# Optimization experiments

Hardware: AMD Instinct MI355X
Metric: run time of the kernel (lower is better)

Reference implementation:

```python
import jax, jax.numpy as jnp
import numpy as np

N_WIRES = 8
DIM = 1 << N_WIRES  # 256
ENC_WIRES = [0, 1, 2, 2, 4, 5, 6, 7]  # faithful to source: wire 2 twice, wire 3 skipped

# Precompute composed CNOT-ring permutation: CNOT(0,1),(1,2),...,(6,7),(7,0)
_idx = np.arange(DIM)
_perm = _idx.copy()
for c, t in [(k, k + 1) for k in range(N_WIRES - 1)] + [(N_WIRES - 1, 0)]:
    cbit = (_idx >> (N_WIRES - 1 - c)) & 1
    P = np.where(cbit == 1, _idx ^ (1 << (N_WIRES - 1 - t)), _idx)
    _perm = _perm[P]
CNOT_PERM = jnp.asarray(_perm)
# Pauli-Z sign table per wire: (8, 256)
Z_SIGNS = jnp.asarray(1 - 2 * ((_idx[None, :] >> (N_WIRES - 1 - np.arange(N_WIRES)[:, None])) & 1)).astype(jnp.float32)


def _rx(state, wire, theta):
    """Apply RX(theta) on `wire`. state: (N, 256) complex64, theta: (N,) float."""
    N = state.shape[0]
    s = state.reshape(N, 1 << wire, 2, 1 << (N_WIRES - 1 - wire))
    half = theta * 0.5
    c = jnp.cos(half)[:, None, None]
    sn = jnp.sin(half)[:, None, None]
    a, b = s[:, :, 0, :], s[:, :, 1, :]
    top = c * a - 1j * sn * b
    bot = -1j * sn * a + c * b
    return jnp.stack([top, bot], axis=2).reshape(N, DIM)


def qlayer(tokens, theta):
    """Batched 8-qubit circuit: encoder RX(x_k), trainable RX(theta_w), CNOT ring, <Z_w>.
    tokens: (N, 8) float32 -> (N, 8) float32 expectation values."""
    N = tokens.shape[0]
    state = jnp.zeros((N, DIM), jnp.complex64).at[:, 0].set(1.0)
    for k, w in enumerate(ENC_WIRES):
        state = _rx(state, w, tokens[:, k])
    for w in range(N_WIRES):
        state = _rx(state, w, jnp.broadcast_to(theta[w], (N,)))
    state = state[:, CNOT_PERM]
    probs = state.real ** 2 + state.imag ** 2  # (N, 256)
    return probs @ Z_SIGNS.T  # (N, 8)


def setup_inputs() -> dict:
    key = jax.random.key(0)
    kx, kt = jax.random.split(key)
    x = jax.random.normal(kx, (16, 1024, 8), dtype=jnp.float32)
    theta = jax.random.uniform(kt, (8,), dtype=jnp.float32, minval=0.0, maxval=2.0 * np.pi)
    return {"x": x, "theta": theta}


def reference(x, theta):
    B, S, E = x.shape
    H, dk = 2, E // 2
    tok = x.reshape(B * S, E)
    # Original computes Q, K, V with the SAME shared q_layer on the SAME input,
    # so Q == K == V; compute once.
    qkv = qlayer(tok, theta).reshape(B, S, E)
    h = qkv.reshape(B, S, H, dk).transpose(0, 2, 1, 3)  # (B,H,S,dk)
    scores = jnp.einsum('bhqd,bhkd->bhqk', h, h) / np.sqrt(dk).astype(np.float32)
    w = jax.nn.softmax(scores, axis=-1)  # (eval mode: dropout inactive)
    attn = jnp.einsum('bhqk,bhkd->bhqd', w, h)
    concat = attn.transpose(0, 2, 1, 3).reshape(B, S, E)
    out = qlayer(concat.reshape(B * S, E), theta).reshape(B, S, E)
    return out
```

## Files before the change

### kernel.cpp

```cpp
#include <hip/hip_runtime.h>

#define SEQ 1024

typedef __attribute__((ext_vector_type(2))) float f2;

static __device__ __forceinline__ int slot_addr(int s) {
    return (s ^ ((s >> 6) & 7)) << 2;
}

static __device__ __forceinline__ void qrow(const float th[8], const float y[8], float o[8]) {
    float a[8];
    a[0] = y[0] + th[0];
    a[1] = y[1] + th[1];
    a[2] = y[2] + y[3] + th[2];
    a[3] = th[3];
    a[4] = y[4] + th[4];
    a[5] = y[5] + th[5];
    a[6] = y[6] + th[6];
    a[7] = y[7] + th[7];
    float c[8];
#pragma unroll
    for (int w = 0; w < 8; ++w) c[w] = __cosf(a[w]);
    o[1] = c[0] * c[1];
#pragma unroll
    for (int w = 2; w < 8; ++w) o[w] = o[w - 1] * c[w];
    float s = c[7];
#pragma unroll
    for (int w = 6; w >= 1; --w) s *= c[w];
    o[0] = s;
}

__global__ __launch_bounds__(256, 4) void mhaq_fused(const float* __restrict__ x,
                                                     const float* __restrict__ theta,
                                                     float* __restrict__ out) {
    __shared__ __align__(16) float smem[8192 + 160];
    float* const res = smem + 8192;

    const int b   = blockIdx.x >> 6;
    const int qof = (blockIdx.x & 63) << 4;
    const int t   = threadIdx.x;

    float th[8];
#pragma unroll
    for (int w = 0; w < 8; ++w) th[w] = theta[w];

    const float4* xb = (const float4*)(x + (size_t)b * SEQ * 8);
    float4 v0[4], v1[4];
#pragma unroll
    for (int r = 0; r < 4; ++r) {
        const int k = t + (r << 8);
        v0[r] = xb[2 * k];
        v1[r] = xb[2 * k + 1];
    }
#pragma unroll
    for (int r = 0; r < 4; ++r) {
        const int k = t + (r << 8);
        const float y[8] = {v0[r].x, v0[r].y, v0[r].z, v0[r].w,
                            v1[r].x, v1[r].y, v1[r].z, v1[r].w};
        float o[8];
        qrow(th, y, o);
        *(float4*)&smem[slot_addr(2 * k)]     = make_float4(o[0], o[1], o[2], o[3]);
        *(float4*)&smem[slot_addr(2 * k + 1)] = make_float4(o[4], o[5], o[6], o[7]);
    }
    __syncthreads();

    const int lane = t & 63;
    const int wv   = t >> 6;
    const int g    = lane >> 4;
    const int m    = lane & 15;
    const int q0   = qof + (g << 2);

    const float qscale = 0.5f * 1.44269504f;
    f2 qv[4][4];
#pragma unroll
    for (int qq = 0; qq < 4; ++qq) {
        const float4 qa = *(const float4*)&smem[slot_addr(2 * (q0 + qq))];
        const float4 qb = *(const float4*)&smem[slot_addr(2 * (q0 + qq) + 1)];
        qv[qq][0] = f2{qa.x, qa.y} * qscale;
        qv[qq][1] = f2{qa.z, qa.w} * qscale;
        qv[qq][2] = f2{qb.x, qb.y} * qscale;
        qv[qq][3] = f2{qb.z, qb.w} * qscale;
    }

    float l0[4] = {0.f, 0.f, 0.f, 0.f};
    float l1[4] = {0.f, 0.f, 0.f, 0.f};
    f2 a01[4], a23[4], a45[4], a67[4];
#pragma unroll
    for (int qq = 0; qq < 4; ++qq) {
        a01[qq] = f2{0.f, 0.f};
        a23[qq] = f2{0.f, 0.f};
        a45[qq] = f2{0.f, 0.f};
        a67[qq] = f2{0.f, 0.f};
    }

    const int kbase = (wv << 8) + (m << 4);
#pragma unroll 4
    for (int i = 0; i < 16; ++i) {
        const int s0 = (kbase + i) << 1;
        const float4 k0 = *(const float4*)&smem[slot_addr(s0)];
        const float4 k1 = *(const float4*)&smem[slot_addr(s0 + 1)];
        const f2 k01 = {k0.x, k0.y}, k23 = {k0.z, k0.w};
        const f2 k45 = {k1.x, k1.y}, k67 = {k1.z, k1.w};
#pragma unroll
        for (int qq = 0; qq < 4; ++qq) {
            const f2 d0 = qv[qq][0] * k01 + qv[qq][1] * k23;
            const f2 d1 = qv[qq][2] * k45 + qv[qq][3] * k67;
            const float e0 = __builtin_amdgcn_exp2f(d0.x + d0.y);
            const float e1 = __builtin_amdgcn_exp2f(d1.x + d1.y);
            l0[qq] += e0;
            l1[qq] += e1;
            const f2 e0v = {e0, e0}, e1v = {e1, e1};
            a01[qq] += e0v * k01;
            a23[qq] += e0v * k23;
            a45[qq] += e1v * k45;
            a67[qq] += e1v * k67;
        }
    }

    float buf[40];
#pragma unroll
    for (int qq = 0; qq < 4; ++qq) {
        buf[qq * 10 + 0] = l0[qq];
        buf[qq * 10 + 1] = l1[qq];
        buf[qq * 10 + 2] = a01[qq].x;
        buf[qq * 10 + 3] = a01[qq].y;
        buf[qq * 10 + 4] = a23[qq].x;
        buf[qq * 10 + 5] = a23[qq].y;
        buf[qq * 10 + 6] = a45[qq].x;
        buf[qq * 10 + 7] = a45[qq].y;
        buf[qq * 10 + 8] = a67[qq].x;
        buf[qq * 10 + 9] = a67[qq].y;
    }
#pragma unroll
    for (int i = 0; i < 40; ++i) buf[i] += __shfl_xor(buf[i], 8, 64);

    __syncthreads();

    if (m < 8) {
        const int rid = (wv << 5) + (g << 3) + m;
        float4* pp = (float4*)&smem[rid * 44];
#pragma unroll
        for (int i = 0; i < 10; ++i) pp[i] = ((const float4*)buf)[i];
    }
    __syncthreads();

    if (t < 160) {
        const int q  = t / 10;
        const int j  = t - q * 10;
        const int gg = q >> 2, qq = q & 3;
        float s = 0.f;
#pragma unroll
        for (int w = 0; w < 4; ++w)
#pragma unroll
            for (int mm = 0; mm < 8; ++mm)
                s += smem[((w << 5) + (gg << 3) + mm) * 44 + qq * 10 + j];
        res[q * 10 + j] = s;
    }
    __syncthreads();

    if (t < 16) {
        const float* r = &res[t * 10];
        const float inv0 = 1.0f / r[0];
        const float inv1 = 1.0f / r[1];
        const float y[8] = {r[2] * inv0, r[3] * inv0, r[4] * inv0, r[5] * inv0,
                            r[6] * inv1, r[7] * inv1, r[8] * inv1, r[9] * inv1};
        float o[8];
        qrow(th, y, o);
        float4* op = (float4*)(out + ((size_t)(b * SEQ + qof + t)) * 8);
        op[0] = make_float4(o[0], o[1], o[2], o[3]);
        op[1] = make_float4(o[4], o[5], o[6], o[7]);
    }
}

extern "C" void kernel_launch(void* const* d_in, const int* in_sizes, int n_in,
                              void* d_out, int out_size, void* d_ws, size_t ws_size,
                              hipStream_t stream) {
    const float* x     = (const float*)d_in[0];
    const float* theta = (const float*)d_in[1];
    float* out         = (float*)d_out;
    mhaq_fused<<<dim3(1024), dim3(256), 0, stream>>>(x, theta, out);
}
```

Measured before the change: 67.87 us.

## Split front qlayer into separate kernel and read keys from global memory

Instead of each of the 1024 blocks recomputing the first quantum layer for its whole batch row of 1024 tokens into shared memory, a small front kernel computes it once per token into workspace. The attention kernel then reads keys straight from global memory (L1/L2 cached) and remaps lanes to 2 queries by 8 key partitions, cutting redundant cosine work and the large LDS footprint. The cost is an extra kernel launch, a round trip through global memory, and per-thread global loads in the inner loop instead of LDS reads.

```diff
diff --git a/kernel.cpp b/kernel.cpp
--- a/kernel.cpp
+++ b/kernel.cpp
@@ -3,10 +3,6 @@
 #define SEQ 1024
 
 typedef __attribute__((ext_vector_type(2))) float f2;
-
-static __device__ __forceinline__ int slot_addr(int s) {
-    return (s ^ ((s >> 6) & 7)) << 2;
-}
 
 static __device__ __forceinline__ void qrow(const float th[8], const float y[8], float o[8]) {
     float a[8];
@@ -30,79 +26,74 @@
     o[0] = s;
 }
 
-__global__ __launch_bounds__(256, 4) void mhaq_fused(const float* __restrict__ x,
-                                                     const float* __restrict__ theta,
-                                                     float* __restrict__ out) {
-    __shared__ __align__(16) float smem[8192 + 160];
-    float* const res = smem + 8192;
+__global__ __launch_bounds__(256) void qlayer_front(const float* __restrict__ x,
+                                                    const float* __restrict__ theta,
+                                                    float* __restrict__ h) {
+    const int r = (blockIdx.x << 8) + threadIdx.x;
+    float th[8];
+#pragma unroll
+    for (int w = 0; w < 8; ++w) th[w] = theta[w];
+    const float4 va = ((const float4*)x)[2 * r];
+    const float4 vb = ((const float4*)x)[2 * r + 1];
+    const float y[8] = {va.x, va.y, va.z, va.w, vb.x, vb.y, vb.z, vb.w};
+    float o[8];
+    qrow(th, y, o);
+    ((float4*)h)[2 * r]     = make_float4(o[0], o[1], o[2], o[3]);
+    ((float4*)h)[2 * r + 1] = make_float4(o[4], o[5], o[6], o[7]);
+}
+
+__global__ __launch_bounds__(256, 4) void mhaq_attn(const float* __restrict__ h,
+                                                    const float* __restrict__ theta,
+                                                    float* __restrict__ out) {
+    __shared__ __align__(16) float part[640];
 
     const int b   = blockIdx.x >> 6;
     const int qof = (blockIdx.x & 63) << 4;
     const int t   = threadIdx.x;
+    const int lane = t & 63;
+    const int wv   = t >> 6;
+    const int g    = lane >> 3;
+    const int m    = lane & 7;
+    const int q0   = qof + (g << 1);
 
     float th[8];
 #pragma unroll
     for (int w = 0; w < 8; ++w) th[w] = theta[w];
 
-    const float4* xb = (const float4*)(x + (size_t)b * SEQ * 8);
-    float4 v0[4], v1[4];
-#pragma unroll
-    for (int r = 0; r < 4; ++r) {
-        const int k = t + (r << 8);
-        v0[r] = xb[2 * k];
-        v1[r] = xb[2 * k + 1];
-    }
-#pragma unroll
-    for (int r = 0; r < 4; ++r) {
-        const int k = t + (r << 8);
-        const float y[8] = {v0[r].x, v0[r].y, v0[r].z, v0[r].w,
-                            v1[r].x, v1[r].y, v1[r].z, v1[r].w};
-        float o[8];
-        qrow(th, y, o);
-        *(float4*)&smem[slot_addr(2 * k)]     = make_float4(o[0], o[1], o[2], o[3]);
-        *(float4*)&smem[slot_addr(2 * k + 1)] = make_float4(o[4], o[5], o[6], o[7]);
-    }
-    __syncthreads();
-
-    const int lane = t & 63;
-    const int wv   = t >> 6;
-    const int g    = lane >> 4;
-    const int m    = lane & 15;
-    const int q0   = qof + (g << 2);
+    const float4* hb = (const float4*)(h + (size_t)b * SEQ * 8);
 
     const float qscale = 0.5f * 1.44269504f;
-    f2 qv[4][4];
+    f2 qv[2][4];
 #pragma unroll
-    for (int qq = 0; qq < 4; ++qq) {
-        const float4 qa = *(const float4*)&smem[slot_addr(2 * (q0 + qq))];
-        const float4 qb = *(const float4*)&smem[slot_addr(2 * (q0 + qq) + 1)];
+    for (int qq = 0; qq < 2; ++qq) {
+        const float4 qa = hb[2 * (q0 + qq)];
+        const float4 qb = hb[2 * (q0 + qq) + 1];
         qv[qq][0] = f2{qa.x, qa.y} * qscale;
         qv[qq][1] = f2{qa.z, qa.w} * qscale;
         qv[qq][2] = f2{qb.x, qb.y} * qscale;
         qv[qq][3] = f2{qb.z, qb.w} * qscale;
     }
 
-    float l0[4] = {0.f, 0.f, 0.f, 0.f};
-    float l1[4] = {0.f, 0.f, 0.f, 0.f};
-    f2 a01[4], a23[4], a45[4], a67[4];
+    float l0[2] = {0.f, 0.f};
+    float l1[2] = {0.f, 0.f};
+    f2 a01[2], a23[2], a45[2], a67[2];
 #pragma unroll
-    for (int qq = 0; qq < 4; ++qq) {
+    for (int qq = 0; qq < 2; ++qq) {
         a01[qq] = f2{0.f, 0.f};
         a23[qq] = f2{0.f, 0.f};
         a45[qq] = f2{0.f, 0.f};
         a67[qq] = f2{0.f, 0.f};
     }
 
-    const int kbase = (wv << 8) + (m << 4);
+    const int kbase = (wv << 8) + (m << 5);
 #pragma unroll 4
-    for (int i = 0; i < 16; ++i) {
-        const int s0 = (kbase + i) << 1;
-        const float4 k0 = *(const float4*)&smem[slot_addr(s0)];
-        const float4 k1 = *(const float4*)&smem[slot_addr(s0 + 1)];
+    for (int i = 0; i < 32; ++i) {
+        const float4 k0 = hb[2 * (kbase + i)];
+        const float4 k1 = hb[2 * (kbase + i) + 1];
         const f2 k01 = {k0.x, k0.y}, k23 = {k0.z, k0.w};
         const f2 k45 = {k1.x, k1.y}, k67 = {k1.z, k1.w};
 #pragma unroll
-        for (int qq = 0; qq < 4; ++qq) {
+        for (int qq = 0; qq < 2; ++qq) {
             const f2 d0 = qv[qq][0] * k01 + qv[qq][1] * k23;
             const f2 d1 = qv[qq][2] * k45 + qv[qq][3] * k67;
             const float e0 = __builtin_amdgcn_exp2f(d0.x + d0.y);
@@ -117,9 +108,9 @@
         }
     }
 
-    float buf[40];
+    float buf[20];
 #pragma unroll
-    for (int qq = 0; qq < 4; ++qq) {
+    for (int qq = 0; qq < 2; ++qq) {
         buf[qq * 10 + 0] = l0[qq];
         buf[qq * 10 + 1] = l1[qq];
         buf[qq * 10 + 2] = a01[qq].x;
@@ -132,34 +123,28 @@
         buf[qq * 10 + 9] = a67[qq].y;
     }
 #pragma unroll
-    for (int i = 0; i < 40; ++i) buf[i] += __shfl_xor(buf[i], 8, 64);
+    for (int d = 1; d <= 4; d <<= 1)
+#pragma unroll
+        for (int i = 0; i < 20; ++i) buf[i] += __shfl_xor(buf[i], d, 64);
 
-    __syncthreads();
-
-    if (m < 8) {
-        const int rid = (wv << 5) + (g << 3) + m;
-        float4* pp = (float4*)&smem[rid * 44];
+    if (m == 0) {
+        float4* pp = (float4*)&part[((wv << 3) + g) * 20];
 #pragma unroll
-        for (int i = 0; i < 10; ++i) pp[i] = ((const float4*)buf)[i];
-    }
-    __syncthreads();
-
-    if (t < 160) {
-        const int q  = t / 10;
-        const int j  = t - q * 10;
-        const int gg = q >> 2, qq = q & 3;
-        float s = 0.f;
-#pragma unroll
-        for (int w = 0; w < 4; ++w)
-#pragma unroll
-            for (int mm = 0; mm < 8; ++mm)
-                s += smem[((w << 5) + (gg << 3) + mm) * 44 + qq * 10 + j];
-        res[q * 10 + j] = s;
+        for (int i = 0; i < 5; ++i) pp[i] = ((const float4*)buf)[i];
     }
     __syncthreads();
 
     if (t < 16) {
-        const float* r = &res[t * 10];
+        const int g2 = t >> 1, qq = t & 1;
+        float r[10];
+#pragma unroll
+        for (int j = 0; j < 10; ++j) {
+            float s = 0.f;
+#pragma unroll
+            for (int w = 0; w < 4; ++w)
+                s += part[((w << 3) + g2) * 20 + qq * 10 + j];
+            r[j] = s;
+        }
         const float inv0 = 1.0f / r[0];
         const float inv1 = 1.0f / r[1];
         const float y[8] = {r[2] * inv0, r[3] * inv0, r[4] * inv0, r[5] * inv0,
@@ -178,5 +163,7 @@
     const float* x     = (const float*)d_in[0];
     const float* theta = (const float*)d_in[1];
     float* out         = (float*)d_out;
-    mhaq_fused<<<dim3(1024), dim3(256), 0, stream>>>(x, theta, out);
+    float* h           = (float*)d_ws;
+    qlayer_front<<<dim3(64), dim3(256), 0, stream>>>(x, theta, h);
+    mhaq_attn<<<dim3(1024), dim3(256), 0, stream>>>(h, theta, out);
 }
```

Result: slower. 88.21 us (+30.0%).

## Contiguous per-lane key ranges, shuffle-tree reduction, fewer block barriers

Applied to the files above, without the earlier changes.

Each lane now processes a contiguous 32-slot key range with a new swizzle pattern, and the vectorized f2 arithmetic is replaced by scalar FMA chains. The cross-lane reduction becomes a 3-step xor shuffle tree, so only 2 lanes per 16-group write partials to a dedicated shared buffer. The separate 160-thread reduction pass and two barriers are removed, leaving the final 16 threads to sum 8 partials each. This adds serial summation work in the final threads and forgoes packed-FP32 math.

```diff
diff --git a/kernel.cpp b/kernel.cpp
--- a/kernel.cpp
+++ b/kernel.cpp
@@ -2,10 +2,8 @@
 
 #define SEQ 1024
 
-typedef __attribute__((ext_vector_type(2))) float f2;
-
 static __device__ __forceinline__ int slot_addr(int s) {
-    return (s ^ ((s >> 6) & 7)) << 2;
+    return (s ^ ((s >> 5) & 7)) << 2;
 }
 
 static __device__ __forceinline__ void qrow(const float th[8], const float y[8], float o[8]) {
@@ -33,8 +31,8 @@
 __global__ __launch_bounds__(256, 4) void mhaq_fused(const float* __restrict__ x,
                                                      const float* __restrict__ theta,
                                                      float* __restrict__ out) {
-    __shared__ __align__(16) float smem[8192 + 160];
-    float* const res = smem + 8192;
+    __shared__ __align__(16) float smem[8192 + 1280];
+    float* const part = smem + 8192;
 
     const int b   = blockIdx.x >> 6;
     const int qof = (blockIdx.x & 63) << 4;
@@ -71,95 +69,83 @@
     const int q0   = qof + (g << 2);
 
     const float qscale = 0.5f * 1.44269504f;
-    f2 qv[4][4];
+    float qv[4][8];
 #pragma unroll
     for (int qq = 0; qq < 4; ++qq) {
         const float4 qa = *(const float4*)&smem[slot_addr(2 * (q0 + qq))];
         const float4 qb = *(const float4*)&smem[slot_addr(2 * (q0 + qq) + 1)];
-        qv[qq][0] = f2{qa.x, qa.y} * qscale;
-        qv[qq][1] = f2{qa.z, qa.w} * qscale;
-        qv[qq][2] = f2{qb.x, qb.y} * qscale;
-        qv[qq][3] = f2{qb.z, qb.w} * qscale;
+        qv[qq][0] = qa.x * qscale; qv[qq][1] = qa.y * qscale;
+        qv[qq][2] = qa.z * qscale; qv[qq][3] = qa.w * qscale;
+        qv[qq][4] = qb.x * qscale; qv[qq][5] = qb.y * qscale;
+        qv[qq][6] = qb.z * qscale; qv[qq][7] = qb.w * qscale;
     }
 
-    float l0[4] = {0.f, 0.f, 0.f, 0.f};
-    float l1[4] = {0.f, 0.f, 0.f, 0.f};
-    f2 a01[4], a23[4], a45[4], a67[4];
+    float acc[4][10];
 #pragma unroll
-    for (int qq = 0; qq < 4; ++qq) {
-        a01[qq] = f2{0.f, 0.f};
-        a23[qq] = f2{0.f, 0.f};
-        a45[qq] = f2{0.f, 0.f};
-        a67[qq] = f2{0.f, 0.f};
-    }
+    for (int qq = 0; qq < 4; ++qq)
+#pragma unroll
+        for (int j = 0; j < 10; ++j) acc[qq][j] = 0.f;
 
-    const int kbase = (wv << 8) + (m << 4);
+    const int sbase = (wv << 9) + (m << 5);
 #pragma unroll 4
     for (int i = 0; i < 16; ++i) {
-        const int s0 = (kbase + i) << 1;
+        const int s0 = sbase + (i << 1);
         const float4 k0 = *(const float4*)&smem[slot_addr(s0)];
         const float4 k1 = *(const float4*)&smem[slot_addr(s0 + 1)];
-        const f2 k01 = {k0.x, k0.y}, k23 = {k0.z, k0.w};
-        const f2 k45 = {k1.x, k1.y}, k67 = {k1.z, k1.w};
 #pragma unroll
         for (int qq = 0; qq < 4; ++qq) {
-            const f2 d0 = qv[qq][0] * k01 + qv[qq][1] * k23;
-            const f2 d1 = qv[qq][2] * k45 + qv[qq][3] * k67;
-            const float e0 = __builtin_amdgcn_exp2f(d0.x + d0.y);
-            const float e1 = __builtin_amdgcn_exp2f(d1.x + d1.y);
-            l0[qq] += e0;
-            l1[qq] += e1;
-            const f2 e0v = {e0, e0}, e1v = {e1, e1};
-            a01[qq] += e0v * k01;
-            a23[qq] += e0v * k23;
-            a45[qq] += e1v * k45;
-            a67[qq] += e1v * k67;
+            const float d0 = fmaf(qv[qq][0], k0.x, fmaf(qv[qq][1], k0.y,
+                             fmaf(qv[qq][2], k0.z, qv[qq][3] * k0.w)));
+            const float d1 = fmaf(qv[qq][4], k1.x, fmaf(qv[qq][5], k1.y,
+                             fmaf(qv[qq][6], k1.z, qv[qq][7] * k1.w)));
+            const float e0 = __builtin_amdgcn_exp2f(d0);
+            const float e1 = __builtin_amdgcn_exp2f(d1);
+            acc[qq][0] += e0;
+            acc[qq][1] += e1;
+            acc[qq][2] = fmaf(e0, k0.x, acc[qq][2]);
+            acc[qq][3] = fmaf(e0, k0.y, acc[qq][3]);
+            acc[qq][4] = fmaf(e0, k0.z, acc[qq][4]);
+            acc[qq][5] = fmaf(e0, k0.w, acc[qq][5]);
+            acc[qq][6] = fmaf(e1, k1.x, acc[qq][6]);
+            acc[qq][7] = fmaf(e1, k1.y, acc[qq][7]);
+            acc[qq][8] = fmaf(e1, k1.z, acc[qq][8]);
+            acc[qq][9] = fmaf(e1, k1.w, acc[qq][9]);
         }
     }
 
-    float buf[40];
+    float* const accf = &acc[0][0];
 #pragma unroll
-    for (int qq = 0; qq < 4; ++qq) {
-        buf[qq * 10 + 0] = l0[qq];
-        buf[qq * 10 + 1] = l1[qq];
-        buf[qq * 10 + 2] = a01[qq].x;
-        buf[qq * 10 + 3] = a01[qq].y;
-        buf[qq * 10 + 4] = a23[qq].x;
-        buf[qq * 10 + 5] = a23[qq].y;
-        buf[qq * 10 + 6] = a45[qq].x;
-        buf[qq * 10 + 7] = a45[qq].y;
-        buf[qq * 10 + 8] = a67[qq].x;
-        buf[qq * 10 + 9] = a67[qq].y;
+    for (int j = 0; j < 40; ++j) {
+        float v = accf[j];
+        v += __shfl_xor(v, 1, 64);
+        v += __shfl_xor(v, 2, 64);
+        v += __shfl_xor(v, 4, 64);
+        accf[j] = v;
     }
+
+    if ((m & 7) == 0) {
+        const int rid = (((wv << 2) + g) << 1) + (m >> 3);
+        float4* pp = (float4*)&part[rid * 40];
 #pragma unroll
-    for (int i = 0; i < 40; ++i) buf[i] += __shfl_xor(buf[i], 8, 64);
-
-    __syncthreads();
-
-    if (m < 8) {
-        const int rid = (wv << 5) + (g << 3) + m;
-        float4* pp = (float4*)&smem[rid * 44];
-#pragma unroll
-        for (int i = 0; i < 10; ++i) pp[i] = ((const float4*)buf)[i];
-    }
-    __syncthreads();
-
-    if (t < 160) {
-        const int q  = t / 10;
-        const int j  = t - q * 10;
-        const int gg = q >> 2, qq = q & 3;
-        float s = 0.f;
-#pragma unroll
-        for (int w = 0; w < 4; ++w)
-#pragma unroll
-            for (int mm = 0; mm < 8; ++mm)
-                s += smem[((w << 5) + (gg << 3) + mm) * 44 + qq * 10 + j];
-        res[q * 10 + j] = s;
+        for (int i = 0; i < 10; ++i)
+            pp[i] = make_float4(accf[4 * i], accf[4 * i + 1],
+                                accf[4 * i + 2], accf[4 * i + 3]);
     }
     __syncthreads();
 
     if (t < 16) {
-        const float* r = &res[t * 10];
+        const int g2 = t >> 2, qq = t & 3;
+        float r[10];
+#pragma unroll
+        for (int j = 0; j < 10; ++j) {
+            float s = 0.f;
+#pragma unroll
+            for (int w = 0; w < 4; ++w)
+#pragma unroll
+                for (int hb = 0; hb < 2; ++hb)
+                    s += part[(((((w << 2) + g2) << 1) + hb) * 40) + qq * 10 + j];
+            r[j] = s;
+        }
         const float inv0 = 1.0f / r[0];
         const float inv1 = 1.0f / r[1];
         const float y[8] = {r[2] * inv0, r[3] * inv0, r[4] * inv0, r[5] * inv0,
```

Measured after the change: 70.18 us. 1.03x slower.
